# Performance work log

Measured on AMD Instinct MI355X. Metric: run time of the kernel, lower is better.

Reference implementation:

```python
import jax, jax.numpy as jnp
import numpy as np


def setup_inputs() -> dict:
    key = jax.random.key(0)
    k1, k2 = jax.random.split(key)
    H = W = 4096
    input1 = jax.random.normal(k1, (1, 1, H, W), dtype=jnp.float32)   # moving image
    input2 = jax.random.normal(k2, (1, 2, H, W), dtype=jnp.float32)   # dense flow (dH, dW)
    return {"input1": input1, "input2": input2}


def reference(input1, input2):
    # input1: [B=1, C=1, H, W] image; input2: [B=1, 2, H, W] displacement field
    B, C, H, W = input1.shape
    f32 = jnp.float32

    # identity mesh (matches torch.linspace outer-product construction)
    h_mesh = jnp.broadcast_to(jnp.arange(H, dtype=f32)[None, :, None], (B, H, W))
    w_mesh = jnp.broadcast_to(jnp.arange(W, dtype=f32)[None, None, :], (B, H, W))

    # warped sampling coordinates, shifted by +1 for the zero-padding border
    H_up = (input2[:, 0] + h_mesh).reshape(-1) + 1.0   # [B*H*W]
    W_up = (input2[:, 1] + w_mesh).reshape(-1) + 1.0

    # zero-pad image by 1 pixel on each spatial side
    img = jnp.pad(input1, ((0, 0), (0, 0), (1, 1), (1, 1)))  # [B, C, H+2, W+2]
    Hp, Wp = H + 2, W + 2

    hf = jnp.floor(H_up).astype(jnp.int32)
    hc = hf + 1
    wf = jnp.floor(W_up).astype(jnp.int32)
    wc = wf + 1
    hf = jnp.clip(hf, 0, Hp - 1)
    hc = jnp.clip(hc, 0, Hp - 1)
    wf = jnp.clip(wf, 0, Wp - 1)
    wc = jnp.clip(wc, 0, Wp - 1)

    img_flat = img.reshape(-1)  # B = C = 1
    val_000 = img_flat[hf * Wp + wf]
    val_010 = img_flat[hc * Wp + wf]
    val_001 = img_flat[hf * Wp + wc]
    val_011 = img_flat[hc * Wp + wc]

    dH = hc.astype(f32) - H_up
    dW = wc.astype(f32) - W_up
    out = (val_000 * (dW * dH)
           + val_010 * (dW * (1.0 - dH))
           + val_001 * ((1.0 - dW) * dH)
           + val_011 * ((1.0 - dW) * (1.0 - dH)))

    # [B*H*W] -> [B, H, W, C] -> [B, C, H, W]
    return out.reshape(B, H, W, C).transpose(0, 3, 1, 2)
```

## Files before the change

### kernel.cpp

```cpp
#include <hip/hip_runtime.h>


#define IMG_H 4096
#define IMG_W 4096
#define TR 16
#define TC 128
#define HALO 8
#define SR (TR + 2 * HALO)
#define SC (TC + 2 * HALO)
#define SC4 (SC / 4)
#define NCHUNK (SR * SC4)
#define KT 4
#define BTR (TR * KT)
#define NTY (IMG_H / TR)

typedef float f2  __attribute__((ext_vector_type(2)));
typedef float f2u __attribute__((ext_vector_type(2), aligned(4)));
typedef float f4  __attribute__((ext_vector_type(4)));

__device__ __forceinline__ float full_pixel(const float* __restrict__ img,
                                            float fhv, float fwv, int h, int w)
{
    float Hu = (fhv + (float)h) + 1.0f;
    float Wu = (fwv + (float)w) + 1.0f;

    int hf = (int)floorf(Hu);
    int wf = (int)floorf(Wu);
    int hc = hf + 1;
    int wc = wf + 1;

    int hfc = min(max(hf, 0), IMG_H + 1);
    int hcc = min(max(hc, 0), IMG_H + 1);
    int wfc = min(max(wf, 0), IMG_W + 1);
    int wcc = min(max(wc, 0), IMG_W + 1);

    float dH = (float)hcc - Hu;
    float dW = (float)wcc - Wu;

    int rf = hfc - 1, rc = hcc - 1, cf = wfc - 1, cc = wcc - 1;
    bool rf_in = (unsigned)rf < IMG_H;
    bool rc_in = (unsigned)rc < IMG_H;
    bool cf_in = (unsigned)cf < IMG_W;
    bool cc_in = (unsigned)cc < IMG_W;

    int rf_cl = min(max(rf, 0), IMG_H - 1);
    int rc_cl = min(max(rc, 0), IMG_H - 1);
    int cf_cl = min(max(cf, 0), IMG_W - 1);
    int cc_cl = min(max(cc, 0), IMG_W - 1);
    int cb    = min(max(cf, 0), IMG_W - 2);

    int sf = cf_cl - cb;
    int sc = cc_cl - cb;

    float A = dW * dH;
    float B = dW * (1.0f - dH);
    float C = (1.0f - dW) * dH;
    float D = (1.0f - dW) * (1.0f - dH);
    float w00 = (rf_in && cf_in) ? A : 0.0f;
    float w10 = (rc_in && cf_in) ? B : 0.0f;
    float w01 = (rf_in && cc_in) ? C : 0.0f;
    float w11 = (rc_in && cc_in) ? D : 0.0f;

    float a0x = (sf ? 0.0f : w00) + (sc ? 0.0f : w01);
    float a0y = (sf ? w00 : 0.0f) + (sc ? w01 : 0.0f);
    float a1x = (sf ? 0.0f : w10) + (sc ? 0.0f : w11);
    float a1y = (sf ? w10 : 0.0f) + (sc ? w11 : 0.0f);

    f2u p0 = *(const f2u*)(img + (rf_cl << 12) + cb);
    f2u p1 = *(const f2u*)(img + (rc_cl << 12) + cb);
    return p0.x * a0x + p0.y * a0y + p1.x * a1x + p1.y * a1y;
}

__global__ __launch_bounds__(256) void warp_bilinear_kernel(
    const float* __restrict__ img,
    const float* __restrict__ flow,
    float* __restrict__ out)
{
    __shared__ float tile[2][SR * SC];

    const int HW   = IMG_H * IMG_W;
    const int tid  = threadIdx.x;
    const int lane = tid & 63;
    const int wv   = tid >> 6;
    const int bx   = blockIdx.x, by = blockIdx.y;
    const int w0   = bx * TC + lane * 2;
    const int c_lo = bx * TC - HALO;

    if (bx == 0 || bx == (int)gridDim.x - 1) {
        #pragma unroll
        for (int t = 0; t < KT; ++t) {
            const int h0 = by * BTR + t * TR + wv * 4;
            int rowidx[4]; f2 fh[4], fw[4];
            #pragma unroll
            for (int r = 0; r < 4; ++r)
                rowidx[r] = (h0 + r) * IMG_W + w0;
            #pragma unroll
            for (int r = 0; r < 4; ++r)
                fh[r] = __builtin_nontemporal_load((const f2*)(flow + rowidx[r]));
            #pragma unroll
            for (int r = 0; r < 4; ++r)
                fw[r] = __builtin_nontemporal_load((const f2*)(flow + HW + rowidx[r]));
            #pragma unroll
            for (int r = 0; r < 4; ++r) {
                f2 res;
                #pragma unroll
                for (int c = 0; c < 2; ++c)
                    res[c] = full_pixel(img, fh[r][c], fw[r][c], h0 + r, w0 + c);
                __builtin_nontemporal_store(res, (f2*)(out + rowidx[r]));
            }
        }
        return;
    }

    int  sg_i[5], sg_m[5];
    bool sg_on[5];
    #pragma unroll
    for (int it = 0; it < 5; ++it) {
        int t = tid + it * 256;
        sg_on[it] = (t < NCHUNK);
        sg_i[it]  = t / SC4;
        sg_m[it]  = (t - sg_i[it] * SC4) * 4;
    }

    const int  ty0  = by * KT;
    const bool tb_f = (ty0 == 0);
    const bool tb_l = (ty0 + KT - 1 == NTY - 1);

    auto stage = [&](int buf, int t) {
        const int r_lo = by * BTR + t * TR - HALO;
        #pragma unroll
        for (int it = 0; it < 5; ++it)
            if (sg_on[it]) {
                f4 v = *(const f4*)(img + (r_lo + sg_i[it]) * IMG_W
                                       + (c_lo + sg_m[it]));
                *(f4*)(&tile[buf][sg_i[it] * SC + sg_m[it]]) = v;
            }
    };

    f2  FH[2][4], FW[2][4];
    int RI[2][4];
    auto flowload = [&](int buf, int t) {
        const int h0 = by * BTR + t * TR + wv * 4;
        #pragma unroll
        for (int r = 0; r < 4; ++r)
            RI[buf][r] = (h0 + r) * IMG_W + w0;
        #pragma unroll
        for (int r = 0; r < 4; ++r)
            FH[buf][r] = __builtin_nontemporal_load((const f2*)(flow + RI[buf][r]));
        #pragma unroll
        for (int r = 0; r < 4; ++r)
            FW[buf][r] = __builtin_nontemporal_load((const f2*)(flow + HW + RI[buf][r]));
    };

    if (!tb_f) stage(0, 0);
    flowload(0, 0);
    __syncthreads();

    #pragma unroll
    for (int t = 0; t < KT; ++t) {
        const int cur = t & 1;

        if (t + 1 < KT) {
            const bool nb = (t + 1 == KT - 1) && tb_l;
            if (!nb) stage(cur ^ 1, t + 1);
            flowload(cur ^ 1, t + 1);
        }

        const bool thisb = (t == 0 && tb_f) || (t == KT - 1 && tb_l);
        const int  h0    = by * BTR + t * TR + wv * 4;

        if (thisb) {
            #pragma unroll
            for (int r = 0; r < 4; ++r) {
                f2 res;
                #pragma unroll
                for (int c = 0; c < 2; ++c)
                    res[c] = full_pixel(img, FH[cur][r][c], FW[cur][r][c],
                                        h0 + r, w0 + c);
                __builtin_nontemporal_store(res, (f2*)(out + RI[cur][r]));
            }
        } else {
            const int r_lo  = by * BTR + t * TR - HALO;
            const int rbase = -1 - r_lo;
            const int cbase = -1 - c_lo;

            int   li0[4][2];
            float A_[4][2], B_[4][2], C_[4][2], D_[4][2];
            bool  ok = true;

            #pragma unroll
            for (int r = 0; r < 4; ++r) {
                #pragma unroll
                for (int c = 0; c < 2; ++c) {
                    float Hu = (FH[cur][r][c] + (float)(h0 + r)) + 1.0f;
                    float Wu = (FW[cur][r][c] + (float)(w0 + c)) + 1.0f;

                    int hf = (int)floorf(Hu);
                    int wf = (int)floorf(Wu);
                    float dH = (float)(hf + 1) - Hu;
                    float dW = (float)(wf + 1) - Wu;

                    int i0 = hf + rbase;
                    int jb = wf + cbase;
                    ok = ok && ((unsigned)i0 < SR - 1) && ((unsigned)jb < SC - 1);
                    li0[r][c] = i0 * SC + jb;

                    float omH = 1.0f - dH, omW = 1.0f - dW;
                    A_[r][c] = dW * dH;
                    C_[r][c] = omW * dH;
                    B_[r][c] = dW * omH;
                    D_[r][c] = omW * omH;
                }
            }

            float res[4][2];
            if (__builtin_expect(ok, 1)) {
                float q0x[4][2], q0y[4][2], q1x[4][2], q1y[4][2];
                #pragma unroll
                for (int r = 0; r < 4; ++r)
                    #pragma unroll
                    for (int c = 0; c < 2; ++c) {
                        q0x[r][c] = tile[cur][li0[r][c]];
                        q0y[r][c] = tile[cur][li0[r][c] + 1];
                        q1x[r][c] = tile[cur][li0[r][c] + SC];
                        q1y[r][c] = tile[cur][li0[r][c] + SC + 1];
                    }
                #pragma unroll
                for (int r = 0; r < 4; ++r)
                    #pragma unroll
                    for (int c = 0; c < 2; ++c)
                        res[r][c] = q0x[r][c] * A_[r][c] + q0y[r][c] * C_[r][c]
                                  + q1x[r][c] * B_[r][c] + q1y[r][c] * D_[r][c];
            }
            if (__builtin_expect(!ok, 0)) {
                #pragma unroll
                for (int r = 0; r < 4; ++r)
                    #pragma unroll
                    for (int c = 0; c < 2; ++c)
                        res[r][c] = full_pixel(img, FH[cur][r][c], FW[cur][r][c],
                                               h0 + r, w0 + c);
            }

            #pragma unroll
            for (int r = 0; r < 4; ++r) {
                f2 v; v[0] = res[r][0]; v[1] = res[r][1];
                __builtin_nontemporal_store(v, (f2*)(out + RI[cur][r]));
            }
        }

        if (t + 1 < KT) __syncthreads();
    }
}

extern "C" void kernel_launch(void* const* d_in, const int* in_sizes, int n_in,
                              void* d_out, int out_size, void* d_ws, size_t ws_size,
                              hipStream_t stream) {
    const float* img  = (const float*)d_in[0];
    const float* flow = (const float*)d_in[1];
    float* out = (float*)d_out;

    dim3 grid(IMG_W / TC, IMG_H / BTR);
    dim3 block(256);
    warp_bilinear_kernel<<<grid, block, 0, stream>>>(img, flow, out);
}
```

Baseline: 260.6 us.

## Register-stage next image tile to overlap loads and unify border handling

The next tile's global image loads now go into registers before the current tile is computed, and are written to shared memory only after the compute finishes. This lets the load latency overlap with the bilinear arithmetic instead of stalling on a load-then-store at issue time. Border blocks and border tiles no longer take separate full-gather paths. Staging clamps coordinates, and an added in-image bounds check routes edge pixels to the fallback path. This costs extra registers for the staged vectors and adds compares per pixel.

```diff
diff --git a/kernel.cpp b/kernel.cpp
--- a/kernel.cpp
+++ b/kernel.cpp
@@ -12,7 +12,6 @@
 #define NCHUNK (SR * SC4)
 #define KT 4
 #define BTR (TR * KT)
-#define NTY (IMG_H / TR)
 
 typedef float f2  __attribute__((ext_vector_type(2)));
 typedef float f2u __attribute__((ext_vector_type(2), aligned(4)));
@@ -78,41 +77,16 @@
 {
     __shared__ float tile[2][SR * SC];
 
-    const int HW   = IMG_H * IMG_W;
-    const int tid  = threadIdx.x;
-    const int lane = tid & 63;
-    const int wv   = tid >> 6;
-    const int bx   = blockIdx.x, by = blockIdx.y;
-    const int w0   = bx * TC + lane * 2;
-    const int c_lo = bx * TC - HALO;
-
-    if (bx == 0 || bx == (int)gridDim.x - 1) {
-        #pragma unroll
-        for (int t = 0; t < KT; ++t) {
-            const int h0 = by * BTR + t * TR + wv * 4;
-            int rowidx[4]; f2 fh[4], fw[4];
-            #pragma unroll
-            for (int r = 0; r < 4; ++r)
-                rowidx[r] = (h0 + r) * IMG_W + w0;
-            #pragma unroll
-            for (int r = 0; r < 4; ++r)
-                fh[r] = __builtin_nontemporal_load((const f2*)(flow + rowidx[r]));
-            #pragma unroll
-            for (int r = 0; r < 4; ++r)
-                fw[r] = __builtin_nontemporal_load((const f2*)(flow + HW + rowidx[r]));
-            #pragma unroll
-            for (int r = 0; r < 4; ++r) {
-                f2 res;
-                #pragma unroll
-                for (int c = 0; c < 2; ++c)
-                    res[c] = full_pixel(img, fh[r][c], fw[r][c], h0 + r, w0 + c);
-                __builtin_nontemporal_store(res, (f2*)(out + rowidx[r]));
-            }
-        }
-        return;
-    }
-
-    int  sg_i[5], sg_m[5];
+    const int HW    = IMG_H * IMG_W;
+    const int tid   = threadIdx.x;
+    const int lane  = tid & 63;
+    const int wv    = tid >> 6;
+    const int bx    = blockIdx.x, by = blockIdx.y;
+    const int w0    = bx * TC + lane * 2;
+    const int c_lo  = bx * TC - HALO;
+    const int cbase = -1 - c_lo;
+
+    int  sg_i[5], sg_m[5], sg_c[5];
     bool sg_on[5];
     #pragma unroll
     for (int it = 0; it < 5; ++it) {
@@ -120,26 +94,29 @@
         sg_on[it] = (t < NCHUNK);
         sg_i[it]  = t / SC4;
         sg_m[it]  = (t - sg_i[it] * SC4) * 4;
+        sg_c[it]  = min(max(c_lo + sg_m[it], 0), IMG_W - 4);
     }
 
-    const int  ty0  = by * KT;
-    const bool tb_f = (ty0 == 0);
-    const bool tb_l = (ty0 + KT - 1 == NTY - 1);
-
-    auto stage = [&](int buf, int t) {
+    f4  S[5];
+    f2  FH[2][4], FW[2][4];
+    int RI[2][4];
+
+    auto stage_load = [&](int t) {
         const int r_lo = by * BTR + t * TR - HALO;
         #pragma unroll
         for (int it = 0; it < 5; ++it)
             if (sg_on[it]) {
-                f4 v = *(const f4*)(img + (r_lo + sg_i[it]) * IMG_W
-                                       + (c_lo + sg_m[it]));
-                *(f4*)(&tile[buf][sg_i[it] * SC + sg_m[it]]) = v;
+                int gr = min(max(r_lo + sg_i[it], 0), IMG_H - 1);
+                S[it] = *(const f4*)(img + gr * IMG_W + sg_c[it]);
             }
     };
-
-    f2  FH[2][4], FW[2][4];
-    int RI[2][4];
-    auto flowload = [&](int buf, int t) {
+    auto stage_write = [&](int buf) {
+        #pragma unroll
+        for (int it = 0; it < 5; ++it)
+            if (sg_on[it])
+                *(f4*)(&tile[buf][sg_i[it] * SC + sg_m[it]]) = S[it];
+    };
+    auto flow_load = [&](int buf, int t) {
         const int h0 = by * BTR + t * TR + wv * 4;
         #pragma unroll
         for (int r = 0; r < 4; ++r)
@@ -152,8 +129,9 @@
             FW[buf][r] = __builtin_nontemporal_load((const f2*)(flow + HW + RI[buf][r]));
     };
 
-    if (!tb_f) stage(0, 0);
-    flowload(0, 0);
+    stage_load(0);
+    flow_load(0, 0);
+    stage_write(0);
     __syncthreads();
 
     #pragma unroll
@@ -161,94 +139,85 @@
         const int cur = t & 1;
 
         if (t + 1 < KT) {
-            const bool nb = (t + 1 == KT - 1) && tb_l;
-            if (!nb) stage(cur ^ 1, t + 1);
-            flowload(cur ^ 1, t + 1);
-        }
-
-        const bool thisb = (t == 0 && tb_f) || (t == KT - 1 && tb_l);
-        const int  h0    = by * BTR + t * TR + wv * 4;
-
-        if (thisb) {
-            #pragma unroll
-            for (int r = 0; r < 4; ++r) {
-                f2 res;
+            stage_load(t + 1);
+            flow_load(cur ^ 1, t + 1);
+        }
+
+        const int h0    = by * BTR + t * TR + wv * 4;
+        const int r_lo  = by * BTR + t * TR - HALO;
+        const int rbase = -1 - r_lo;
+
+        int   li0[4][2];
+        float A_[4][2], B_[4][2], C_[4][2], D_[4][2];
+        bool  ok = true;
+
+        #pragma unroll
+        for (int r = 0; r < 4; ++r) {
+            #pragma unroll
+            for (int c = 0; c < 2; ++c) {
+                float Hu = (FH[cur][r][c] + (float)(h0 + r)) + 1.0f;
+                float Wu = (FW[cur][r][c] + (float)(w0 + c)) + 1.0f;
+
+                int hf = (int)floorf(Hu);
+                int wf = (int)floorf(Wu);
+                float dH = (float)(hf + 1) - Hu;
+                float dW = (float)(wf + 1) - Wu;
+
+                int i0 = hf + rbase;
+                int jb = wf + cbase;
+
+                ok = ok && ((unsigned)(hf - 1) < IMG_H - 1)
+                        && ((unsigned)(wf - 1) < IMG_W - 1)
+                        && ((unsigned)i0 < SR - 1)
+                        && ((unsigned)jb < SC - 1);
+                li0[r][c] = i0 * SC + jb;
+
+                float omH = 1.0f - dH, omW = 1.0f - dW;
+                A_[r][c] = dW * dH;
+                C_[r][c] = omW * dH;
+                B_[r][c] = dW * omH;
+                D_[r][c] = omW * omH;
+            }
+        }
+
+        float res[4][2];
+        if (__builtin_expect(ok, 1)) {
+            float q0x[4][2], q0y[4][2], q1x[4][2], q1y[4][2];
+            #pragma unroll
+            for (int r = 0; r < 4; ++r)
+                #pragma unroll
+                for (int c = 0; c < 2; ++c) {
+                    q0x[r][c] = tile[cur][li0[r][c]];
+                    q0y[r][c] = tile[cur][li0[r][c] + 1];
+                    q1x[r][c] = tile[cur][li0[r][c] + SC];
+                    q1y[r][c] = tile[cur][li0[r][c] + SC + 1];
+                }
+            #pragma unroll
+            for (int r = 0; r < 4; ++r)
                 #pragma unroll
                 for (int c = 0; c < 2; ++c)
-                    res[c] = full_pixel(img, FH[cur][r][c], FW[cur][r][c],
-                                        h0 + r, w0 + c);
-                __builtin_nontemporal_store(res, (f2*)(out + RI[cur][r]));
-            }
-        } else {
-            const int r_lo  = by * BTR + t * TR - HALO;
-            const int rbase = -1 - r_lo;
-            const int cbase = -1 - c_lo;
-
-            int   li0[4][2];
-            float A_[4][2], B_[4][2], C_[4][2], D_[4][2];
-            bool  ok = true;
-
-            #pragma unroll
-            for (int r = 0; r < 4; ++r) {
+                    res[r][c] = q0x[r][c] * A_[r][c] + q0y[r][c] * C_[r][c]
+                              + q1x[r][c] * B_[r][c] + q1y[r][c] * D_[r][c];
+        }
+        if (__builtin_expect(!ok, 0)) {
+            #pragma unroll
+            for (int r = 0; r < 4; ++r)
                 #pragma unroll
-                for (int c = 0; c < 2; ++c) {
-                    float Hu = (FH[cur][r][c] + (float)(h0 + r)) + 1.0f;
-                    float Wu = (FW[cur][r][c] + (float)(w0 + c)) + 1.0f;
-
-                    int hf = (int)floorf(Hu);
-                    int wf = (int)floorf(Wu);
-                    float dH = (float)(hf + 1) - Hu;
-                    float dW = (float)(wf + 1) - Wu;
-
-                    int i0 = hf + rbase;
-                    int jb = wf + cbase;
-                    ok = ok && ((unsigned)i0 < SR - 1) && ((unsigned)jb < SC - 1);
-                    li0[r][c] = i0 * SC + jb;
-
-                    float omH = 1.0f - dH, omW = 1.0f - dW;
-                    A_[r][c] = dW * dH;
-                    C_[r][c] = omW * dH;
-                    B_[r][c] = dW * omH;
-                    D_[r][c] = omW * omH;
-                }
-            }
-
-            float res[4][2];
-            if (__builtin_expect(ok, 1)) {
-                float q0x[4][2], q0y[4][2], q1x[4][2], q1y[4][2];
-                #pragma unroll
-                for (int r = 0; r < 4; ++r)
-                    #pragma unroll
-                    for (int c = 0; c < 2; ++c) {
-                        q0x[r][c] = tile[cur][li0[r][c]];
-                        q0y[r][c] = tile[cur][li0[r][c] + 1];
-                        q1x[r][c] = tile[cur][li0[r][c] + SC];
-                        q1y[r][c] = tile[cur][li0[r][c] + SC + 1];
-                    }
-                #pragma unroll
-                for (int r = 0; r < 4; ++r)
-                    #pragma unroll
-                    for (int c = 0; c < 2; ++c)
-                        res[r][c] = q0x[r][c] * A_[r][c] + q0y[r][c] * C_[r][c]
-                                  + q1x[r][c] * B_[r][c] + q1y[r][c] * D_[r][c];
-            }
-            if (__builtin_expect(!ok, 0)) {
-                #pragma unroll
-                for (int r = 0; r < 4; ++r)
-                    #pragma unroll
-                    for (int c = 0; c < 2; ++c)
-                        res[r][c] = full_pixel(img, FH[cur][r][c], FW[cur][r][c],
-                                               h0 + r, w0 + c);
-            }
-
-            #pragma unroll
-            for (int r = 0; r < 4; ++r) {
-                f2 v; v[0] = res[r][0]; v[1] = res[r][1];
-                __builtin_nontemporal_store(v, (f2*)(out + RI[cur][r]));
-            }
-        }
-
-        if (t + 1 < KT) __syncthreads();
+                for (int c = 0; c < 2; ++c)
+                    res[r][c] = full_pixel(img, FH[cur][r][c], FW[cur][r][c],
+                                           h0 + r, w0 + c);
+        }
+
+        #pragma unroll
+        for (int r = 0; r < 4; ++r) {
+            f2 v; v[0] = res[r][0]; v[1] = res[r][1];
+            __builtin_nontemporal_store(v, (f2*)(out + RI[cur][r]));
+        }
+
+        if (t + 1 < KT) {
+            stage_write(cur ^ 1);
+            __syncthreads();
+        }
     }
 }
 
```

Measured after the change: 254.1 us. 2.5% less time.
